# Kernel optimization log

Hardware: AMD Instinct MI355X
Metric: run time of the kernel (lower is better)

## Reference

```python
import jax, jax.numpy as jnp
import numpy as np

N_HEAD = 16


def _rope_cache(T, head_dim):
    half = head_dim // 2
    inv_freq = 1.0 / (10000.0 ** (jnp.arange(half, dtype=jnp.float32) / half))
    t = jnp.arange(T, dtype=jnp.float32)
    freqs = jnp.einsum('i,j->ij', t, inv_freq)            # (T, half)
    cos = jnp.repeat(jnp.cos(freqs), 2, axis=-1)          # (T, head_dim)
    sin = jnp.repeat(jnp.sin(freqs), 2, axis=-1)
    return cos, sin


def _apply_rope(x, cos, sin):
    # x: (B, H, T, D); cos/sin: (T, D)
    x1 = x[..., ::2]
    x2 = x[..., 1::2]
    x_rot = jnp.stack([-x2, x1], axis=-1).reshape(x.shape)
    return x * cos[None, None] + x_rot * sin[None, None]


def setup_inputs() -> dict:
    key = jax.random.key(0)
    k1, k2, k3 = jax.random.split(key, 3)
    B, T, C = 2, 2048, 1024
    x = jax.random.normal(k1, (B, T, C), dtype=jnp.float32)
    Wqkv = jax.random.normal(k2, (C, 3 * C), dtype=jnp.float32) * 0.02
    Wo = jax.random.normal(k3, (C, C), dtype=jnp.float32) * 0.02
    bo = jnp.zeros((C,), dtype=jnp.float32)
    return {"x": x, "Wqkv": Wqkv, "Wo": Wo, "bo": bo}


def reference(x, Wqkv, Wo, bo):
    B, T, C = x.shape
    H = N_HEAD
    D = C // H
    scale = D ** -0.5

    qkv = x @ Wqkv                                        # (B, T, 3C)
    qkv = qkv.reshape(B, T, 3, H, D).transpose(2, 0, 3, 1, 4)  # (3, B, H, T, D)
    q, k, v = qkv[0], qkv[1], qkv[2]

    cos, sin = _rope_cache(T, D)
    q = _apply_rope(q, cos, sin)
    k = _apply_rope(k, cos, sin)

    att = jnp.einsum('bhqd,bhkd->bhqk', q, k) * scale     # (B, H, T, T)
    causal = jnp.tril(jnp.ones((T, T), dtype=bool))
    att = jnp.where(causal[None, None], att, -jnp.inf)
    att = jax.nn.softmax(att, axis=-1)                    # dropout is identity in eval

    out = jnp.einsum('bhqk,bhkd->bhqd', att, v)           # (B, H, T, D)
    out = out.transpose(0, 2, 1, 3).reshape(B, T, C)
    return out @ Wo + bo
```

## Files before the change

### kernel.cpp

```cpp
#include <hip/hip_runtime.h>

typedef __attribute__((ext_vector_type(8))) short bf16x8;
typedef __attribute__((ext_vector_type(4))) float f32x4;
typedef __attribute__((ext_vector_type(4))) unsigned uint32x4;

#define MFMA32(a, b, c) __builtin_amdgcn_mfma_f32_16x16x32_bf16((a), (b), (c), 0, 0, 0)

__device__ __forceinline__ unsigned short f2bf(float f) {
  unsigned u = __builtin_bit_cast(unsigned, f);
  u += 0x7fffu + ((u >> 16) & 1u);
  return (unsigned short)(u >> 16);
}
__device__ __forceinline__ unsigned pack2(float a, float b) {
  return (unsigned)f2bf(a) | ((unsigned)f2bf(b) << 16);
}
__device__ __forceinline__ unsigned pack2t(float lo, float hi) {
  return __builtin_amdgcn_perm(__builtin_bit_cast(unsigned, hi),
                               __builtin_bit_cast(unsigned, lo), 0x07060302u);
}
__device__ __forceinline__ void gl_lds16(const unsigned short* g, unsigned short* l) {
  __builtin_amdgcn_global_load_lds(
      (const __attribute__((address_space(1))) unsigned int*)(g),
      (__attribute__((address_space(3))) unsigned int*)(l), 16, 0, 0);
}

#define QSCALE 0.18033688011112042f

__global__ __launch_bounds__(256) void prep_kernel(
    const float* __restrict__ x, const float* __restrict__ Wqkv,
    const float* __restrict__ Wo, unsigned short* __restrict__ xb,
    unsigned short* __restrict__ wqt, unsigned short* __restrict__ wot) {
  __shared__ unsigned short Tl[64][72];
  const int bid = blockIdx.x, tid = threadIdx.x;
  if (bid < 2048) {
    int i = (bid * 256 + tid) * 8;
    float4 a = *(const float4*)(x + i);
    float4 b = *(const float4*)(x + i + 4);
    uint4 w;
    w.x = pack2(a.x, a.y); w.y = pack2(a.z, a.w);
    w.z = pack2(b.x, b.y); w.w = pack2(b.z, b.w);
    *(uint4*)(xb + i) = w;
  } else {
    const float* src;
    unsigned short* dst;
    int N, kt, nt;
    if (bid < 2816) {
      int r = bid - 2048;
      src = Wqkv; dst = wqt; N = 3072;
      nt = (r % 48) * 64; kt = (r / 48) * 64;
    } else {
      int r = bid - 2816;
      src = Wo; dst = wot; N = 1024;
      nt = (r & 15) * 64; kt = (r >> 4) * 64;
    }
    const int rr = tid >> 2, cs = (tid & 3) * 16;
    const float* sp = src + (kt + rr) * N + nt + cs;
    uint4 w0, w1;
    {
      float4 a = *(const float4*)(sp), b = *(const float4*)(sp + 4);
      float4 c = *(const float4*)(sp + 8), d = *(const float4*)(sp + 12);
      w0.x = pack2(a.x, a.y); w0.y = pack2(a.z, a.w);
      w0.z = pack2(b.x, b.y); w0.w = pack2(b.z, b.w);
      w1.x = pack2(c.x, c.y); w1.y = pack2(c.z, c.w);
      w1.z = pack2(d.x, d.y); w1.w = pack2(d.z, d.w);
    }
    *(uint4*)(&Tl[rr][cs]) = w0;
    *(uint4*)(&Tl[rr][cs + 8]) = w1;
    __syncthreads();
    unsigned short tmp[16];
#pragma unroll
    for (int i = 0; i < 16; i++) tmp[i] = Tl[cs + i][rr];
    unsigned short* dp = dst + (nt + rr) * 1024 + kt + cs;
    *(uint4*)(dp) = *(const uint4*)(&tmp[0]);
    *(uint4*)(dp + 8) = *(const uint4*)(&tmp[8]);
  }
}

__global__ __launch_bounds__(256) void qkv_rope_kernel(
    const unsigned short* __restrict__ xb, const unsigned short* __restrict__ wt,
    unsigned short* __restrict__ qws, unsigned short* __restrict__ kws,
    unsigned short* __restrict__ vws) {
  __shared__ unsigned short Al[2 * 128 * 32];
  __shared__ unsigned short Bl[2 * 128 * 32];

  const int tid = threadIdx.x;
  const int lane = tid & 63, wid = tid >> 6;
  const int quad = lane >> 4, col = lane & 15;
  const int wm = (wid >> 1) * 64, wn = (wid & 1) * 64;
  const int n0 = blockIdx.x * 128, m0 = blockIdx.y * 128;

  f32x4 acc[4][4] = {};
  const int srow = wid * 32 + (lane >> 2);
  const int gseg = ((lane & 3) ^ ((lane >> 3) & 3)) * 8;
  const int fsg = (quad ^ ((col >> 1) & 3)) * 8;

  for (int k0 = 0; k0 < 1024; k0 += 64) {
#pragma unroll
    for (int c = 0; c < 2; c++) {
      const int kc = k0 + c * 32, lo = c * 4096;
      gl_lds16(xb + (m0 + srow) * 1024 + kc + gseg, Al + lo + (wid * 32) * 32);
      gl_lds16(xb + (m0 + srow + 16) * 1024 + kc + gseg,
               Al + lo + (wid * 32 + 16) * 32);
      gl_lds16(wt + (n0 + srow) * 1024 + kc + gseg, Bl + lo + (wid * 32) * 32);
      gl_lds16(wt + (n0 + srow + 16) * 1024 + kc + gseg,
               Bl + lo + (wid * 32 + 16) * 32);
    }
    __syncthreads();

#pragma unroll
    for (int c = 0; c < 2; c++) {
      const int lo = c * 4096;
      bf16x8 af[4], bfr[4];
#pragma unroll
      for (int i = 0; i < 4; i++)
        af[i] = *(const bf16x8*)(&Al[lo + (wm + i * 16 + col) * 32 + fsg]);
#pragma unroll
      for (int j = 0; j < 4; j++)
        bfr[j] = *(const bf16x8*)(&Bl[lo + (wn + j * 16 + col) * 32 + fsg]);
#pragma unroll
      for (int i = 0; i < 4; i++)
#pragma unroll
        for (int j = 0; j < 4; j++)
          acc[i][j] = MFMA32(af[i], bfr[j], acc[i][j]);
    }
    __syncthreads();
  }

#pragma unroll
  for (int i = 0; i < 4; i++) {
#pragma unroll
    for (int j = 0; j < 4; j++) {
      const int nbase = n0 + wn + j * 16;
      const int region = nbase >> 10;
#pragma unroll
      for (int r = 0; r < 4; r++) {
        int m = m0 + wm + i * 16 + quad * 4 + r;
        int n = nbase + col;
        float val = acc[i][j][r];
        int nn = n & 1023, h = nn >> 6, d = nn & 63, b = m >> 11, t = m & 2047;
        if (region < 2) {
          float other = __shfl_xor(val, 1);
          float invf = __expf(-(float)(d >> 1) * 0.28782313662425572f);
          float ang = (float)t * invf;
          float sn, cs;
          __sincosf(ang, &sn, &cs);
          float rot = (d & 1) ? other : -other;
          val = fmaf(val, cs, rot * sn);
        }
        int bh = (b << 4) + h;
        if (region == 0) {
          qws[(bh * 2048 + t) * 64 + d] = f2bf(val * QSCALE);
        } else if (region == 1) {
          kws[(bh * 2048 + t) * 64 + d] = f2bf(val);
        } else {
          int tl = t & 31, g = t >> 5;
          int qd = (tl & 15) >> 2;
          int jj = (tl & 3) + ((tl & 16) ? 4 : 0);
          int tp = g * 32 + qd * 8 + jj;
          vws[(bh * 64 + d) * 2048 + tp] = f2bf(val);
        }
      }
    }
  }
}

__global__ __launch_bounds__(256) void attn_kernel(
    const unsigned short* __restrict__ qws, const unsigned short* __restrict__ kws,
    const unsigned short* __restrict__ vws, unsigned short* __restrict__ aws) {
  __shared__ unsigned short Kl[64 * 64];
  __shared__ unsigned short Vl[64 * 64];

  const int tid = threadIdx.x;
  const int lane = tid & 63, wid = tid >> 6;
  const int quad = lane >> 4, col = lane & 15;
  const int bh = blockIdx.y;
  const unsigned short* qb = qws + bh * (2048 * 64);
  const unsigned short* kb = kws + bh * (2048 * 64);
  const unsigned short* vb = vws + bh * (64 * 2048);
  const int b = bh >> 4, h = bh & 15;

  const int sro = wid * 16 + (lane >> 3);
  const int sgs = ((lane & 7) ^ ((lane >> 3) & 7)) * 8;
  const int sA = (quad ^ (col & 7)) * 8;

#pragma unroll
  for (int pass = 0; pass < 2; pass++) {
    const int q0blk = (pass == 0 ? (int)blockIdx.x : 31 - (int)blockIdx.x) * 64;
    const int qt = q0blk + wid * 16;
    const int qi = qt + col;

    bf16x8 qf0 = *(const bf16x8*)(qb + (qt + col) * 64 + quad * 8);
    bf16x8 qf1 = *(const bf16x8*)(qb + (qt + col) * 64 + 32 + quad * 8);

    f32x4 o[4] = {};
    float lsum = 0.f;

    for (int k0 = 0; k0 < q0blk + 64; k0 += 64) {
      gl_lds16(kb + (k0 + sro) * 64 + sgs, Kl + (wid * 16) * 64);
      gl_lds16(kb + (k0 + sro + 8) * 64 + sgs, Kl + (wid * 16 + 8) * 64);
      gl_lds16(vb + sro * 2048 + k0 + sgs, Vl + (wid * 16) * 64);
      gl_lds16(vb + (sro + 8) * 2048 + k0 + sgs, Vl + (wid * 16 + 8) * 64);
      __syncthreads();

      f32x4 sc[4];
#pragma unroll
      for (int s = 0; s < 4; s++) {
        bf16x8 kfa = *(const bf16x8*)(&Kl[(s * 16 + col) * 64 + sA]);
        bf16x8 kfb = *(const bf16x8*)(&Kl[(s * 16 + col) * 64 + (sA ^ 32)]);
        f32x4 z = {0.f, 0.f, 0.f, 0.f};
        z = MFMA32(kfa, qf0, z);
        z = MFMA32(kfb, qf1, z);
        sc[s] = z;
      }
      if (k0 + 64 > qt) {
#pragma unroll
        for (int s = 0; s < 4; s++)
#pragma unroll
          for (int r = 0; r < 4; r++) {
            int key = k0 + s * 16 + quad * 4 + r;
            if (key > qi) sc[s][r] = -1e30f;
          }
      }
      float p[16];
#pragma unroll
      for (int s = 0; s < 4; s++)
#pragma unroll
        for (int r = 0; r < 4; r++) {
          float e = exp2f(sc[s][r]);
          p[s * 4 + r] = e;
          lsum += e;
        }
      uint32x4 u0, u1;
      u0[0] = pack2t(p[0], p[1]);   u0[1] = pack2t(p[2], p[3]);
      u0[2] = pack2t(p[4], p[5]);   u0[3] = pack2t(p[6], p[7]);
      u1[0] = pack2t(p[8], p[9]);   u1[1] = pack2t(p[10], p[11]);
      u1[2] = pack2t(p[12], p[13]); u1[3] = pack2t(p[14], p[15]);
      bf16x8 pf0 = __builtin_bit_cast(bf16x8, u0);
      bf16x8 pf1 = __builtin_bit_cast(bf16x8, u1);
#pragma unroll
      for (int dt = 0; dt < 4; dt++) {
        bf16x8 vfa = *(const bf16x8*)(&Vl[(dt * 16 + col) * 64 + sA]);
        bf16x8 vfb = *(const bf16x8*)(&Vl[(dt * 16 + col) * 64 + (sA ^ 32)]);
        o[dt] = MFMA32(vfa, pf0, o[dt]);
        o[dt] = MFMA32(vfb, pf1, o[dt]);
      }
      __syncthreads();
    }

    lsum += __shfl_xor(lsum, 16);
    lsum += __shfl_xor(lsum, 32);
    float inv = 1.0f / lsum;
#pragma unroll
    for (int dt = 0; dt < 4; dt++)
#pragma unroll
      for (int r = 0; r < 4; r++) {
        int d = dt * 16 + quad * 4 + r;
        aws[(b * 2048 + qt + col) * 1024 + h * 64 + d] = f2bf(o[dt][r] * inv);
      }
  }
}

__global__ __launch_bounds__(256) void out_proj_kernel(
    const unsigned short* __restrict__ attn, const unsigned short* __restrict__ wot,
    const float* __restrict__ bo, float* __restrict__ out) {
  __shared__ unsigned short Al[2 * 64 * 32];
  __shared__ unsigned short Bl[2 * 128 * 32];

  const int tid = threadIdx.x;
  const int lane = tid & 63, wid = tid >> 6;
  const int quad = lane >> 4, col = lane & 15;
  const int wm = (wid >> 1) * 32, wn = (wid & 1) * 64;
  const int n0 = blockIdx.x * 128, m0 = blockIdx.y * 64;

  f32x4 acc[2][4] = {};
  const int sr = lane >> 2;
  const int gseg = ((lane & 3) ^ ((lane >> 3) & 3)) * 8;
  const int fsg = (quad ^ ((col >> 1) & 3)) * 8;

  for (int k0 = 0; k0 < 1024; k0 += 64) {
#pragma unroll
    for (int c = 0; c < 2; c++) {
      const int kc = k0 + c * 32;
      gl_lds16(attn + (m0 + wid * 16 + sr) * 1024 + kc + gseg,
               Al + c * 2048 + (wid * 16) * 32);
      gl_lds16(wot + (n0 + wid * 32 + sr) * 1024 + kc + gseg,
               Bl + c * 4096 + (wid * 32) * 32);
      gl_lds16(wot + (n0 + wid * 32 + 16 + sr) * 1024 + kc + gseg,
               Bl + c * 4096 + (wid * 32 + 16) * 32);
    }
    __syncthreads();

#pragma unroll
    for (int c = 0; c < 2; c++) {
      bf16x8 af[2], bfr[4];
#pragma unroll
      for (int i = 0; i < 2; i++)
        af[i] = *(const bf16x8*)(&Al[c * 2048 + (wm + i * 16 + col) * 32 + fsg]);
#pragma unroll
      for (int j = 0; j < 4; j++)
        bfr[j] = *(const bf16x8*)(&Bl[c * 4096 + (wn + j * 16 + col) * 32 + fsg]);
#pragma unroll
      for (int i = 0; i < 2; i++)
#pragma unroll
        for (int j = 0; j < 4; j++)
          acc[i][j] = MFMA32(af[i], bfr[j], acc[i][j]);
    }
    __syncthreads();
  }

#pragma unroll
  for (int i = 0; i < 2; i++)
#pragma unroll
    for (int j = 0; j < 4; j++)
#pragma unroll
      for (int r = 0; r < 4; r++) {
        int m = m0 + wm + i * 16 + quad * 4 + r;
        int n = n0 + wn + j * 16 + col;
        out[m * 1024 + n] = acc[i][j][r] + bo[n];
      }
}

extern "C" void kernel_launch(void* const* d_in, const int* in_sizes, int n_in,
                              void* d_out, int out_size, void* d_ws, size_t ws_size,
                              hipStream_t stream) {
  const float* x = (const float*)d_in[0];
  const float* Wqkv = (const float*)d_in[1];
  const float* Wo = (const float*)d_in[2];
  const float* bo = (const float*)d_in[3];
  float* out = (float*)d_out;

  unsigned short* qws = (unsigned short*)d_ws;
  unsigned short* kws = qws + 4194304;
  unsigned short* vws = kws + 4194304;
  unsigned short* xb  = vws + 4194304;
  unsigned short* aws = xb;
  unsigned short* wqt = xb + 4194304;
  unsigned short* wot = wqt + 3145728;

  prep_kernel<<<3072, 256, 0, stream>>>(x, Wqkv, Wo, xb, wqt, wot);
  qkv_rope_kernel<<<dim3(24, 32), 256, 0, stream>>>(xb, wqt, qws, kws, vws);
  attn_kernel<<<dim3(16, 32), 256, 0, stream>>>(qws, kws, vws, aws);
  out_proj_kernel<<<dim3(8, 64), 256, 0, stream>>>(aws, wot, bo, out);
}
```

Before: 208.2 us.

## Shrink QKV GEMM M-tile, double K/V tiles and skip masked blocks in attention

The QKV+RoPE GEMM tile drops from 128x128 to 64x128, doubling the grid to 1536 blocks and adding a launch-bounds occupancy hint. The aim is better CU coverage at the cost of more redundant weight traffic. The attention kernel now loads two 64-key K/V tiles per barrier to halve synchronisation. It also skips per-wave 16-key sub-blocks that lie entirely above the causal diagonal, and skips the second PV MFMA half when it is all zeros. The extra branching may hurt scheduling, and the larger LDS footprint may reduce occupancy.

Result: faster. 200.4 us (-3.7%).

```diff
diff --git a/kernel.cpp b/kernel.cpp
--- a/kernel.cpp
+++ b/kernel.cpp
@@ -76,49 +76,47 @@
   }
 }
 
-__global__ __launch_bounds__(256) void qkv_rope_kernel(
+__global__ __launch_bounds__(256, 6) void qkv_rope_kernel(
     const unsigned short* __restrict__ xb, const unsigned short* __restrict__ wt,
     unsigned short* __restrict__ qws, unsigned short* __restrict__ kws,
     unsigned short* __restrict__ vws) {
-  __shared__ unsigned short Al[2 * 128 * 32];
+  __shared__ unsigned short Al[2 * 64 * 32];
   __shared__ unsigned short Bl[2 * 128 * 32];
 
   const int tid = threadIdx.x;
   const int lane = tid & 63, wid = tid >> 6;
   const int quad = lane >> 4, col = lane & 15;
-  const int wm = (wid >> 1) * 64, wn = (wid & 1) * 64;
-  const int n0 = blockIdx.x * 128, m0 = blockIdx.y * 128;
-
-  f32x4 acc[4][4] = {};
-  const int srow = wid * 32 + (lane >> 2);
+  const int wm = (wid >> 1) * 32, wn = (wid & 1) * 64;
+  const int n0 = blockIdx.x * 128, m0 = blockIdx.y * 64;
+
+  f32x4 acc[2][4] = {};
+  const int srA = wid * 16 + (lane >> 2);
+  const int srB = wid * 32 + (lane >> 2);
   const int gseg = ((lane & 3) ^ ((lane >> 3) & 3)) * 8;
   const int fsg = (quad ^ ((col >> 1) & 3)) * 8;
 
   for (int k0 = 0; k0 < 1024; k0 += 64) {
 #pragma unroll
     for (int c = 0; c < 2; c++) {
-      const int kc = k0 + c * 32, lo = c * 4096;
-      gl_lds16(xb + (m0 + srow) * 1024 + kc + gseg, Al + lo + (wid * 32) * 32);
-      gl_lds16(xb + (m0 + srow + 16) * 1024 + kc + gseg,
-               Al + lo + (wid * 32 + 16) * 32);
-      gl_lds16(wt + (n0 + srow) * 1024 + kc + gseg, Bl + lo + (wid * 32) * 32);
-      gl_lds16(wt + (n0 + srow + 16) * 1024 + kc + gseg,
-               Bl + lo + (wid * 32 + 16) * 32);
+      const int kc = k0 + c * 32;
+      gl_lds16(xb + (m0 + srA) * 1024 + kc + gseg, Al + c * 2048 + (wid * 16) * 32);
+      gl_lds16(wt + (n0 + srB) * 1024 + kc + gseg, Bl + c * 4096 + (wid * 32) * 32);
+      gl_lds16(wt + (n0 + srB + 16) * 1024 + kc + gseg,
+               Bl + c * 4096 + (wid * 32 + 16) * 32);
     }
     __syncthreads();
 
 #pragma unroll
     for (int c = 0; c < 2; c++) {
-      const int lo = c * 4096;
-      bf16x8 af[4], bfr[4];
-#pragma unroll
-      for (int i = 0; i < 4; i++)
-        af[i] = *(const bf16x8*)(&Al[lo + (wm + i * 16 + col) * 32 + fsg]);
+      bf16x8 af[2], bfr[4];
+#pragma unroll
+      for (int i = 0; i < 2; i++)
+        af[i] = *(const bf16x8*)(&Al[c * 2048 + (wm + i * 16 + col) * 32 + fsg]);
 #pragma unroll
       for (int j = 0; j < 4; j++)
-        bfr[j] = *(const bf16x8*)(&Bl[lo + (wn + j * 16 + col) * 32 + fsg]);
-#pragma unroll
-      for (int i = 0; i < 4; i++)
+        bfr[j] = *(const bf16x8*)(&Bl[c * 4096 + (wn + j * 16 + col) * 32 + fsg]);
+#pragma unroll
+      for (int i = 0; i < 2; i++)
 #pragma unroll
         for (int j = 0; j < 4; j++)
           acc[i][j] = MFMA32(af[i], bfr[j], acc[i][j]);
@@ -127,7 +125,7 @@
   }
 
 #pragma unroll
-  for (int i = 0; i < 4; i++) {
+  for (int i = 0; i < 2; i++) {
 #pragma unroll
     for (int j = 0; j < 4; j++) {
       const int nbase = n0 + wn + j * 16;
@@ -167,8 +165,8 @@
 __global__ __launch_bounds__(256) void attn_kernel(
     const unsigned short* __restrict__ qws, const unsigned short* __restrict__ kws,
     const unsigned short* __restrict__ vws, unsigned short* __restrict__ aws) {
-  __shared__ unsigned short Kl[64 * 64];
-  __shared__ unsigned short Vl[64 * 64];
+  __shared__ unsigned short Kl[2][64 * 64];
+  __shared__ unsigned short Vl[2][64 * 64];
 
   const int tid = threadIdx.x;
   const int lane = tid & 63, wid = tid >> 6;
@@ -188,6 +186,8 @@
     const int q0blk = (pass == 0 ? (int)blockIdx.x : 31 - (int)blockIdx.x) * 64;
     const int qt = q0blk + wid * 16;
     const int qi = qt + col;
+    const int qi_max = qt + 15;
+    const int kend = q0blk + 64;
 
     bf16x8 qf0 = *(const bf16x8*)(qb + (qt + col) * 64 + quad * 8);
     bf16x8 qf1 = *(const bf16x8*)(qb + (qt + col) * 64 + 32 + quad * 8);
@@ -195,54 +195,67 @@
     f32x4 o[4] = {};
     float lsum = 0.f;
 
-    for (int k0 = 0; k0 < q0blk + 64; k0 += 64) {
-      gl_lds16(kb + (k0 + sro) * 64 + sgs, Kl + (wid * 16) * 64);
-      gl_lds16(kb + (k0 + sro + 8) * 64 + sgs, Kl + (wid * 16 + 8) * 64);
-      gl_lds16(vb + sro * 2048 + k0 + sgs, Vl + (wid * 16) * 64);
-      gl_lds16(vb + (sro + 8) * 2048 + k0 + sgs, Vl + (wid * 16 + 8) * 64);
+    for (int k0 = 0; k0 < kend; k0 += 128) {
+      const int nsub = (kend - k0 > 64) ? 2 : 1;
+      for (int u = 0; u < nsub; u++) {
+        const int kb0 = k0 + u * 64;
+        gl_lds16(kb + (kb0 + sro) * 64 + sgs, Kl[u] + (wid * 16) * 64);
+        gl_lds16(kb + (kb0 + sro + 8) * 64 + sgs, Kl[u] + (wid * 16 + 8) * 64);
+        gl_lds16(vb + sro * 2048 + kb0 + sgs, Vl[u] + (wid * 16) * 64);
+        gl_lds16(vb + (sro + 8) * 2048 + kb0 + sgs, Vl[u] + (wid * 16 + 8) * 64);
+      }
       __syncthreads();
 
-      f32x4 sc[4];
-#pragma unroll
-      for (int s = 0; s < 4; s++) {
-        bf16x8 kfa = *(const bf16x8*)(&Kl[(s * 16 + col) * 64 + sA]);
-        bf16x8 kfb = *(const bf16x8*)(&Kl[(s * 16 + col) * 64 + (sA ^ 32)]);
-        f32x4 z = {0.f, 0.f, 0.f, 0.f};
-        z = MFMA32(kfa, qf0, z);
-        z = MFMA32(kfb, qf1, z);
-        sc[s] = z;
-      }
-      if (k0 + 64 > qt) {
-#pragma unroll
-        for (int s = 0; s < 4; s++)
-#pragma unroll
-          for (int r = 0; r < 4; r++) {
-            int key = k0 + s * 16 + quad * 4 + r;
-            if (key > qi) sc[s][r] = -1e30f;
+      for (int u = 0; u < nsub; u++) {
+        const int kb0 = k0 + u * 64;
+        if (kb0 > qi_max) break;
+        const int smax = min(4, ((qi_max - kb0) >> 4) + 1);
+        const bool diag = (kb0 + 64 > qt);
+        float p[16];
+#pragma unroll
+        for (int s = 0; s < 4; s++) {
+          if (s < smax) {
+            bf16x8 kfa = *(const bf16x8*)(&Kl[u][(s * 16 + col) * 64 + sA]);
+            bf16x8 kfb = *(const bf16x8*)(&Kl[u][(s * 16 + col) * 64 + (sA ^ 32)]);
+            f32x4 z = {0.f, 0.f, 0.f, 0.f};
+            z = MFMA32(kfa, qf0, z);
+            z = MFMA32(kfb, qf1, z);
+            if (diag) {
+#pragma unroll
+              for (int r = 0; r < 4; r++)
+                if (kb0 + s * 16 + quad * 4 + r > qi) z[r] = -1e30f;
+            }
+#pragma unroll
+            for (int r = 0; r < 4; r++) {
+              float e = exp2f(z[r]);
+              p[s * 4 + r] = e;
+              lsum += e;
+            }
+          } else {
+#pragma unroll
+            for (int r = 0; r < 4; r++) p[s * 4 + r] = 0.f;
           }
-      }
-      float p[16];
-#pragma unroll
-      for (int s = 0; s < 4; s++)
-#pragma unroll
-        for (int r = 0; r < 4; r++) {
-          float e = exp2f(sc[s][r]);
-          p[s * 4 + r] = e;
-          lsum += e;
-        }
-      uint32x4 u0, u1;
-      u0[0] = pack2t(p[0], p[1]);   u0[1] = pack2t(p[2], p[3]);
-      u0[2] = pack2t(p[4], p[5]);   u0[3] = pack2t(p[6], p[7]);
-      u1[0] = pack2t(p[8], p[9]);   u1[1] = pack2t(p[10], p[11]);
-      u1[2] = pack2t(p[12], p[13]); u1[3] = pack2t(p[14], p[15]);
-      bf16x8 pf0 = __builtin_bit_cast(bf16x8, u0);
-      bf16x8 pf1 = __builtin_bit_cast(bf16x8, u1);
-#pragma unroll
-      for (int dt = 0; dt < 4; dt++) {
-        bf16x8 vfa = *(const bf16x8*)(&Vl[(dt * 16 + col) * 64 + sA]);
-        bf16x8 vfb = *(const bf16x8*)(&Vl[(dt * 16 + col) * 64 + (sA ^ 32)]);
-        o[dt] = MFMA32(vfa, pf0, o[dt]);
-        o[dt] = MFMA32(vfb, pf1, o[dt]);
+        }
+        uint32x4 u0;
+        u0[0] = pack2t(p[0], p[1]);   u0[1] = pack2t(p[2], p[3]);
+        u0[2] = pack2t(p[4], p[5]);   u0[3] = pack2t(p[6], p[7]);
+        bf16x8 pf0 = __builtin_bit_cast(bf16x8, u0);
+#pragma unroll
+        for (int dt = 0; dt < 4; dt++) {
+          bf16x8 vfa = *(const bf16x8*)(&Vl[u][(dt * 16 + col) * 64 + sA]);
+          o[dt] = MFMA32(vfa, pf0, o[dt]);
+        }
+        if (smax > 2) {
+          uint32x4 u1;
+          u1[0] = pack2t(p[8], p[9]);   u1[1] = pack2t(p[10], p[11]);
+          u1[2] = pack2t(p[12], p[13]); u1[3] = pack2t(p[14], p[15]);
+          bf16x8 pf1 = __builtin_bit_cast(bf16x8, u1);
+#pragma unroll
+          for (int dt = 0; dt < 4; dt++) {
+            bf16x8 vfb = *(const bf16x8*)(&Vl[u][(dt * 16 + col) * 64 + (sA ^ 32)]);
+            o[dt] = MFMA32(vfb, pf1, o[dt]);
+          }
+        }
       }
       __syncthreads();
     }
@@ -338,7 +351,7 @@
   unsigned short* wot = wqt + 3145728;
 
   prep_kernel<<<3072, 256, 0, stream>>>(x, Wqkv, Wo, xb, wqt, wot);
-  qkv_rope_kernel<<<dim3(24, 32), 256, 0, stream>>>(xb, wqt, qws, kws, vws);
+  qkv_rope_kernel<<<dim3(24, 64), 256, 0, stream>>>(xb, wqt, qws, kws, vws);
   attn_kernel<<<dim3(16, 32), 256, 0, stream>>>(qws, kws, vws, aws);
   out_proj_kernel<<<dim3(8, 64), 256, 0, stream>>>(aws, wot, bo, out);
 }
```
